# Performance work log

Measured on AMD Instinct MI355X. Metric: run time of the kernel, lower is better.

The kernel has to match this reference:

```python
import jax, jax.numpy as jnp
import numpy as np

# DeformConv (RegSeg): offset conv + mask conv (sigmoid) + modulated deformable conv v2
STRIDE = 1
PAD = 1
DIL = 1
G = 1          # deformable_groups
KH, KW = 3, 3


def _conv(x, w, b):
    # standard NCHW conv, stride/pad/dilation of the module
    y = jax.lax.conv_general_dilated(
        x, w, window_strides=(STRIDE, STRIDE),
        padding=((PAD, PAD), (PAD, PAD)), rhs_dilation=(DIL, DIL),
        dimension_numbers=("NCHW", "OIHW", "NCHW"))
    return y + b[None, :, None, None]


def _deform_conv2d(x, offset, mask, w, b):
    # torchvision DeformConv2d (modulated, v2) semantics
    B, C, H, W = x.shape
    O = w.shape[0]
    K = KH * KW
    Ho = (H + 2 * PAD - DIL * (KH - 1) - 1) // STRIDE + 1
    Wo = (W + 2 * PAD - DIL * (KW - 1) - 1) // STRIDE + 1
    Cg = C // G

    # base sampling grid: p0 + p_k
    ky = jnp.repeat(jnp.arange(KH), KW) * DIL            # [K]
    kx = jnp.tile(jnp.arange(KW), KH) * DIL              # [K]
    oy = jnp.arange(Ho) * STRIDE - PAD                   # [Ho]
    ox = jnp.arange(Wo) * STRIDE - PAD                   # [Wo]
    base_y = (ky[:, None, None] + oy[None, :, None]).astype(x.dtype)  # [K,Ho,1]
    base_x = (kx[:, None, None] + ox[None, None, :]).astype(x.dtype)  # [K,1,Wo]

    off = offset.reshape(B, G, K, 2, Ho, Wo)             # channel layout: g, k, (dy,dx)
    py = base_y[None, None] + off[:, :, :, 0]            # [B,G,K,Ho,Wo]
    px = base_x[None, None] + off[:, :, :, 1]
    m = mask.reshape(B, G, K, Ho, Wo)

    imgf = x.reshape(B * G, Cg, H * W)
    y0 = jnp.floor(py).astype(jnp.int32)
    x0 = jnp.floor(px).astype(jnp.int32)
    ly = py - y0.astype(x.dtype)
    lx = px - x0.astype(x.dtype)

    def corner(iy, ix, wgt):
        # zero-padded bilinear corner: out-of-bounds corners contribute 0
        valid = (iy >= 0) & (iy < H) & (ix >= 0) & (ix < W)
        idx = (jnp.clip(iy, 0, H - 1) * W + jnp.clip(ix, 0, W - 1)).reshape(B * G, -1)
        g = jax.vmap(lambda im, ii: im[:, ii])(imgf, idx)            # [B*G,Cg,K*Ho*Wo]
        g = g.reshape(B, G, Cg, K, Ho, Wo)
        return g * (wgt * valid.astype(x.dtype))[:, :, None]          # [B,G,Cg,K,Ho,Wo]

    val = (corner(y0,     x0,     (1 - ly) * (1 - lx))
         + corner(y0,     x0 + 1, (1 - ly) * lx)
         + corner(y0 + 1, x0,     ly * (1 - lx))
         + corner(y0 + 1, x0 + 1, ly * lx))
    val = val * m[:, :, None]                                         # modulation

    wr = w.reshape(O, G, Cg, K)
    out = jnp.einsum("bgckpq,ogck->bopq", val, wr) + b[None, :, None, None]
    return out


def setup_inputs() -> dict:
    key = jax.random.key(0)
    ks = jax.random.split(key, 8)
    B, C, H, W, O = 4, 128, 96, 96, 128
    K = KH * KW
    fan = 1.0 / np.sqrt(C * K)
    return {
        "x":        jax.random.normal(ks[0], (B, C, H, W), jnp.float32),
        "x2":       jax.random.normal(ks[1], (B, C, H, W), jnp.float32),
        "offset_w": jax.random.normal(ks[2], (2 * G * K, C, KH, KW), jnp.float32) * 0.01,
        "offset_b": jax.random.normal(ks[3], (2 * G * K,), jnp.float32) * 0.01,
        "mask_w":   jax.random.normal(ks[4], (G * K, C, KH, KW), jnp.float32) * 0.05,
        "mask_b":   jnp.zeros((G * K,), jnp.float32),
        "deform_w": jax.random.normal(ks[5], (O, C, KH, KW), jnp.float32) * fan,
        "deform_b": jax.random.normal(ks[6], (O,), jnp.float32) * fan,
    }


def reference(x, x2, offset_w, offset_b, mask_w, mask_b, deform_w, deform_b):
    offset = _conv(x2, offset_w, offset_b)
    mask = jax.nn.sigmoid(_conv(x2, mask_w, mask_b))
    return _deform_conv2d(x, offset, mask, deform_w, deform_b)
```

## Files before the change

### kernel.cpp

```cpp
#include <hip/hip_runtime.h>

#define CIN   128
#define HH    96
#define WW    96
#define OUTC  128
#define HWSZ  9216
#define KK    9
#define KTOT  1152

typedef __bf16 bf16x8 __attribute__((ext_vector_type(8)));
typedef float  f32x4  __attribute__((ext_vector_type(4)));

__device__ __forceinline__ unsigned short f2bf(float f) {
  unsigned u = __builtin_bit_cast(unsigned, f);
  u += 0x7fffu + ((u >> 16) & 1u);
  return (unsigned short)(u >> 16);
}
__device__ __forceinline__ float bf2f_lo(unsigned w) {
  unsigned u = w << 16;
  return __builtin_bit_cast(float, u);
}
__device__ __forceinline__ float bf2f_hi(unsigned w) {
  unsigned u = w & 0xffff0000u;
  return __builtin_bit_cast(float, u);
}
__device__ __forceinline__ unsigned pack_bf(float v0, float v1) {
  unsigned u0 = __builtin_bit_cast(unsigned, v0) + 0x8000u;
  unsigned u1 = __builtin_bit_cast(unsigned, v1) + 0x8000u;
  return __builtin_amdgcn_perm(u1, u0, 0x07060302u);
}

#define WT2B_O 147456
#define BIAS_O 184320
#define XN_O   184384
#define X2N_O  (184384 + 4718592)

__global__ __launch_bounds__(256) void prep_all(
    const float* __restrict__ x, const float* __restrict__ x2,
    const float* __restrict__ offw, const float* __restrict__ maskw,
    const float* __restrict__ defw, const float* __restrict__ offb,
    const float* __restrict__ maskb, void* __restrict__ wsv) {
  int bid = blockIdx.x;
  int t = threadIdx.x;
  if (bid < 1152) {
    __shared__ unsigned short tile[64][138];
    int tsel = bid / 576;
    int rem = bid - tsel * 576;
    int b = rem / 144;
    int hw0 = (rem % 144) * 64;
    const float* src = tsel ? x2 : x;
    unsigned short* dst = (unsigned short*)wsv + (tsel ? X2N_O : XN_O);
    int px = t & 63, cg = t >> 6;
#pragma unroll
    for (int q = 0; q < 16; ++q) {
      int c = cg * 32 + 2 * q;
      float f0 = src[((size_t)(b * CIN + c))     * HWSZ + hw0 + px];
      float f1 = src[((size_t)(b * CIN + c + 1)) * HWSZ + hw0 + px];
      *(unsigned*)&tile[px][c] = pack_bf(f0, f1);
    }
    __syncthreads();
    unsigned* drow = (unsigned*)(dst + ((size_t)(b * HWSZ + hw0)) * 128);
#pragma unroll
    for (int k = 0; k < 16; ++k) {
      int e = t + 256 * k;
      int pxx = e >> 6, j = e & 63;
      unsigned v = *(const unsigned*)&tile[pxx][2 * j];
      drow[(size_t)pxx * 64 + j] = v;
    }
    return;
  }
  unsigned short* wtb  = (unsigned short*)wsv;
  unsigned short* wt2b = wtb + WT2B_O;
  float* bias32 = (float*)(wtb + BIAS_O);
  int idx = (bid - 1152) * 256 + t;
  if (idx < OUTC * KTOT) {
    int o = idx / KTOT, r = idx - o * KTOT;
    int c = r / KK, tap = r - c * KK;
    wtb[o * KTOT + tap * 128 + c] = f2bf(defw[idx]);
  } else if (idx < OUTC * KTOT + 32 * KTOT) {
    int j = idx - OUTC * KTOT;
    int oc = j / KTOT, r = j - oc * KTOT;
    int c = r / KK, tap = r - c * KK;
    float v = 0.f;
    if (oc < 18)      v = offw[j];
    else if (oc < 27) v = maskw[j - 18 * KTOT];
    wt2b[oc * KTOT + tap * 128 + c] = f2bf(v);
  } else if (idx < OUTC * KTOT + 32 * KTOT + 32) {
    int j = idx - OUTC * KTOT - 32 * KTOT;
    float v = 0.f;
    if (j < 18) v = offb[j]; else if (j < 27) v = maskb[j - 18];
    bias32[j] = v;
  }
}

__global__ __launch_bounds__(256, 3) void fused(
    const float* __restrict__ defb, const void* __restrict__ wsv,
    float* __restrict__ out) {
  const unsigned short* wtb  = (const unsigned short*)wsv;
  const unsigned short* wt2b = wtb + WT2B_O;
  const float* bias32 = (const float*)(wtb + BIAS_O);
  const unsigned short* xn  = wtb + XN_O;
  const unsigned short* x2n = wtb + X2N_O;

  __shared__ unsigned bw[64 * 68];
  __shared__ unsigned short val[64][136];
  __shared__ float om[32][68];
  __shared__ unsigned sidxw[KK * 4 * 64];

  int t = threadIdx.x;
  int w = t >> 6;
  int l15 = t & 15, quad = (t >> 4) & 3;
  int rb = blockIdx.x;
  int bid = (rb & 7) * 72 + (rb >> 3);
  int b = bid / 144;
  int pblk = (bid % 144) * 64;

  int phg[4], pwg[4];
#pragma unroll
  for (int G = 0; G < 4; ++G) {
    int p = pblk + w * 16 + G * 4 + quad;
    phg[G] = p / WW;
    pwg[G] = p - phg[G] * WW;
  }

  f32x4 oa0 = {0.f, 0.f, 0.f, 0.f};
  f32x4 oa1 = {0.f, 0.f, 0.f, 0.f};
  const unsigned short* x2nb = x2n + ((size_t)b * HWSZ) * 128;
  for (int tap = 0; tap < KK; ++tap) {
    int ky = tap / 3 - 1, kx = tap % 3 - 1;
    uint4 vG[4];
#pragma unroll
    for (int G = 0; G < 4; ++G) {
      int y = phg[G] + ky, xx = pwg[G] + kx;
      bool ok = ((unsigned)y < HH) && ((unsigned)xx < WW);
      int pos = ok ? (y * WW + xx) : 0;
      uint4 v = *(const uint4*)(x2nb + ((size_t)pos << 7) + l15 * 8);
      vG[G] = ok ? v : make_uint4(0u, 0u, 0u, 0u);
    }
#pragma unroll
    for (int j = 0; j < 2; ++j) {
      int cc = t + 256 * j;
      int row = cc >> 4, c16 = cc & 15;
      *(uint4*)&bw[row * 68 + c16 * 4] =
          *(const uint4*)(wt2b + (size_t)row * KTOT + tap * 128 + c16 * 8);
    }
#pragma unroll
    for (int G = 0; G < 4; ++G)
      *(uint4*)&val[w * 16 + G * 4 + quad][l15 * 8] = vG[G];
    __syncthreads();
#pragma unroll
    for (int ks = 0; ks < 4; ++ks) {
      bf16x8 af = *(const bf16x8*)&val[w * 16 + l15][ks * 32 + quad * 8];
      bf16x8 b0 = *(const bf16x8*)&bw[(size_t)l15 * 68 + ks * 16 + quad * 4];
      bf16x8 b1 = *(const bf16x8*)&bw[(size_t)(l15 + 16) * 68 + ks * 16 + quad * 4];
      oa0 = __builtin_amdgcn_mfma_f32_16x16x32_bf16(af, b0, oa0, 0, 0, 0);
      oa1 = __builtin_amdgcn_mfma_f32_16x16x32_bf16(af, b1, oa1, 0, 0, 0);
    }
    __syncthreads();
  }
#pragma unroll
  for (int nt = 0; nt < 2; ++nt) {
    f32x4 a = nt ? oa1 : oa0;
    int oc = nt * 16 + l15;
    float bia = bias32[oc];
#pragma unroll
    for (int r = 0; r < 4; ++r)
      om[oc][w * 16 + quad * 4 + r] = a[r] + bia;
  }
  __syncthreads();

  for (int e = t; e < KK * 64; e += 256) {
    int tap = e >> 6, pp = e & 63;
    int gp2 = pblk + pp;
    int h = gp2 / WW, ww_ = gp2 % WW;
    float dy = om[2 * tap][pp], dx = om[2 * tap + 1][pp];
    float mr = om[18 + tap][pp];
    float m = 1.f / (1.f + __expf(-mr));
    float py  = (float)(h + tap / 3 - 1) + dy;
    float pxx = (float)(ww_ + tap % 3 - 1) + dx;
    float y0f = floorf(py), x0f = floorf(pxx);
    int y0 = (int)y0f, x0 = (int)x0f;
    float ly = py - y0f, lx = pxx - x0f;
    int y1 = y0 + 1, x1 = x0 + 1;
    bool vy0 = (unsigned)y0 < HH, vy1 = (unsigned)y1 < HH;
    bool vx0 = (unsigned)x0 < WW, vx1 = (unsigned)x1 < WW;
    int cy0 = min(max(y0, 0), HH - 1), cy1 = min(max(y1, 0), HH - 1);
    int cx0 = min(max(x0, 0), WW - 1), cx1 = min(max(x1, 0), WW - 1);
    unsigned i00 = cy0 * WW + cx0, i01 = cy0 * WW + cx1;
    unsigned i10 = cy1 * WW + cx0, i11 = cy1 * WW + cx1;
    float w00 = (vy0 && vx0) ? m * (1.f - ly) * (1.f - lx) : 0.f;
    float w01 = (vy0 && vx1) ? m * (1.f - ly) * lx         : 0.f;
    float w10 = (vy1 && vx0) ? m * ly * (1.f - lx)         : 0.f;
    float w11 = (vy1 && vx1) ? m * ly * lx                 : 0.f;
    sidxw[(tap * 4 + 0) * 64 + pp] = i00 | ((unsigned)f2bf(w00) << 16);
    sidxw[(tap * 4 + 1) * 64 + pp] = i01 | ((unsigned)f2bf(w01) << 16);
    sidxw[(tap * 4 + 2) * 64 + pp] = i10 | ((unsigned)f2bf(w10) << 16);
    sidxw[(tap * 4 + 3) * 64 + pp] = i11 | ((unsigned)f2bf(w11) << 16);
  }
  __syncthreads();

  f32x4 acc[8];
#pragma unroll
  for (int nt = 0; nt < 8; ++nt) acc[nt] = (f32x4){0.f, 0.f, 0.f, 0.f};
  const unsigned short* xnb = xn + ((size_t)b * HWSZ) * 128;

  for (int tap = 0; tap < KK; ++tap) {
    unsigned sw[4][4];
#pragma unroll
    for (int cr = 0; cr < 4; ++cr)
#pragma unroll
      for (int G = 0; G < 4; ++G)
        sw[cr][G] = sidxw[(tap * 4 + cr) * 64 + w * 16 + G * 4 + quad];
    uint4 v[4][4];
#pragma unroll
    for (int G = 0; G < 4; ++G)
#pragma unroll
      for (int cr = 0; cr < 4; ++cr)
        v[cr][G] = *(const uint4*)(xnb + ((size_t)(sw[cr][G] & 0xffffu) << 7) + l15 * 8);
#pragma unroll
    for (int G = 0; G < 4; ++G) {
      float f[8];
#pragma unroll
      for (int j = 0; j < 8; ++j) f[j] = 0.f;
#pragma unroll
      for (int cr = 0; cr < 4; ++cr) {
        float wc = bf2f_hi(sw[cr][G]);
        const unsigned* a = (const unsigned*)&v[cr][G];
#pragma unroll
        for (int j = 0; j < 4; ++j) {
          f[2 * j]     += wc * bf2f_lo(a[j]);
          f[2 * j + 1] += wc * bf2f_hi(a[j]);
        }
      }
      unsigned od[4];
#pragma unroll
      for (int j = 0; j < 4; ++j) od[j] = pack_bf(f[2 * j], f[2 * j + 1]);
      *(uint4*)&val[w * 16 + G * 4 + quad][l15 * 8] =
          make_uint4(od[0], od[1], od[2], od[3]);
    }
#pragma unroll
    for (int j = 0; j < 4; ++j) {
      int cc = t + 256 * j;
      int row = cc >> 4, c16 = cc & 15;
      *(uint4*)&bw[row * 68 + c16 * 4] =
          *(const uint4*)(wtb + (size_t)row * KTOT + tap * 128 + c16 * 8);
    }
    __syncthreads();
    bf16x8 af[4];
#pragma unroll
    for (int ks = 0; ks < 4; ++ks)
      af[ks] = *(const bf16x8*)&val[w * 16 + l15][ks * 32 + quad * 8];
#pragma unroll
    for (int ks = 0; ks < 4; ++ks)
#pragma unroll
      for (int nt = 0; nt < 4; ++nt) {
        bf16x8 bb = *(const bf16x8*)&bw[(size_t)(nt * 16 + l15) * 68 + ks * 16 + quad * 4];
        acc[nt] = __builtin_amdgcn_mfma_f32_16x16x32_bf16(af[ks], bb, acc[nt], 0, 0, 0);
      }
    __syncthreads();
#pragma unroll
    for (int j = 0; j < 4; ++j) {
      int cc = t + 256 * j;
      int row = cc >> 4, c16 = cc & 15;
      *(uint4*)&bw[row * 68 + c16 * 4] =
          *(const uint4*)(wtb + (size_t)(64 + row) * KTOT + tap * 128 + c16 * 8);
    }
    __syncthreads();
#pragma unroll
    for (int ks = 0; ks < 4; ++ks)
#pragma unroll
      for (int nt = 0; nt < 4; ++nt) {
        bf16x8 bb = *(const bf16x8*)&bw[(size_t)(nt * 16 + l15) * 68 + ks * 16 + quad * 4];
        acc[4 + nt] = __builtin_amdgcn_mfma_f32_16x16x32_bf16(af[ks], bb, acc[4 + nt], 0, 0, 0);
      }
    __syncthreads();
  }

  for (int r = 0; r < 4; ++r) {
    f32x4 a0 = acc[2 * r], a1 = acc[2 * r + 1];
    float db0 = defb[r * 32 + l15];
    float db1 = defb[r * 32 + 16 + l15];
    if (r) __syncthreads();
#pragma unroll
    for (int reg = 0; reg < 4; ++reg) {
      om[l15]     [w * 16 + quad * 4 + reg] = a0[reg] + db0;
      om[16 + l15][w * 16 + quad * 4 + reg] = a1[reg] + db1;
    }
    __syncthreads();
    int row = t >> 4;
    int col4 = (t & 15) * 4;
#pragma unroll
    for (int hrow = 0; hrow < 2; ++hrow) {
      int rr = row + hrow * 16;
      float4 vv = *(float4*)&om[rr][col4];
      *(float4*)&out[((size_t)b * OUTC + r * 32 + rr) * HWSZ + pblk + col4] = vv;
    }
  }
}

extern "C" void kernel_launch(void* const* d_in, const int* in_sizes, int n_in,
                              void* d_out, int out_size, void* d_ws, size_t ws_size,
                              hipStream_t stream) {
  const float* x     = (const float*)d_in[0];
  const float* x2    = (const float*)d_in[1];
  const float* offw  = (const float*)d_in[2];
  const float* offb  = (const float*)d_in[3];
  const float* maskw = (const float*)d_in[4];
  const float* maskb = (const float*)d_in[5];
  const float* defw  = (const float*)d_in[6];
  const float* defb  = (const float*)d_in[7];
  float* out = (float*)d_out;

  hipLaunchKernelGGL(prep_all, dim3(1873), dim3(256), 0, stream,
                     x, x2, offw, maskw, defw, offb, maskb, d_ws);
  hipLaunchKernelGGL(fused, dim3(576), dim3(256), 0, stream, defb, d_ws, out);
}
```

Measured before the change: 145.5 us.

## Pre-swizzle weights into MFMA fragment order and load B directly from global

The prep kernel now stores the deform and offset/mask weights in a layout that matches the MFMA B-operand fragment, so each lane reads its bf16x8 straight from global memory (via L1/L2) instead of staging weights through shared memory. This removes the bw LDS buffer, its store loops and several __syncthreads per tap in both the offset conv and the deform GEMM. The val tile is padded to 144 columns. The tradeoff is more global/L2 load traffic per wave, since each of the 4 waves reloads the same weights, with latency exposed directly ahead of the MFMAs. Freeing the LDS could raise occupancy.

```diff
diff --git a/kernel.cpp b/kernel.cpp
--- a/kernel.cpp
+++ b/kernel.cpp
@@ -30,7 +30,7 @@
   return __builtin_amdgcn_perm(u1, u0, 0x07060302u);
 }
 
-#define WT2B_O 147456
+#define WT2T_O 147456
 #define BIAS_O 184320
 #define XN_O   184384
 #define X2N_O  (184384 + 4718592)
@@ -69,22 +69,28 @@
     }
     return;
   }
-  unsigned short* wtb  = (unsigned short*)wsv;
-  unsigned short* wt2b = wtb + WT2B_O;
-  float* bias32 = (float*)(wtb + BIAS_O);
+  unsigned short* wtt  = (unsigned short*)wsv;
+  unsigned short* wt2t = wtt + WT2T_O;
+  float* bias32 = (float*)(wtt + BIAS_O);
   int idx = (bid - 1152) * 256 + t;
   if (idx < OUTC * KTOT) {
     int o = idx / KTOT, r = idx - o * KTOT;
     int c = r / KK, tap = r - c * KK;
-    wtb[o * KTOT + tap * 128 + c] = f2bf(defw[idx]);
+    int nt = o >> 4, l15o = o & 15;
+    int ks = c >> 5, quad = (c >> 3) & 3, j = c & 7;
+    wtt[(size_t)(((tap * 4 + ks) * 8 + nt) * 64 + quad * 16 + l15o) * 8 + j] =
+        f2bf(defw[idx]);
   } else if (idx < OUTC * KTOT + 32 * KTOT) {
-    int j = idx - OUTC * KTOT;
-    int oc = j / KTOT, r = j - oc * KTOT;
+    int jj = idx - OUTC * KTOT;
+    int oc = jj / KTOT, r = jj - oc * KTOT;
     int c = r / KK, tap = r - c * KK;
     float v = 0.f;
-    if (oc < 18)      v = offw[j];
-    else if (oc < 27) v = maskw[j - 18 * KTOT];
-    wt2b[oc * KTOT + tap * 128 + c] = f2bf(v);
+    if (oc < 18)      v = offw[jj];
+    else if (oc < 27) v = maskw[jj - 18 * KTOT];
+    int nt2 = oc >> 4, l15o = oc & 15;
+    int ks = c >> 5, quad = (c >> 3) & 3, j = c & 7;
+    wt2t[(size_t)(((tap * 4 + ks) * 2 + nt2) * 64 + quad * 16 + l15o) * 8 + j] =
+        f2bf(v);
   } else if (idx < OUTC * KTOT + 32 * KTOT + 32) {
     int j = idx - OUTC * KTOT - 32 * KTOT;
     float v = 0.f;
@@ -96,20 +102,20 @@
 __global__ __launch_bounds__(256, 3) void fused(
     const float* __restrict__ defb, const void* __restrict__ wsv,
     float* __restrict__ out) {
-  const unsigned short* wtb  = (const unsigned short*)wsv;
-  const unsigned short* wt2b = wtb + WT2B_O;
-  const float* bias32 = (const float*)(wtb + BIAS_O);
-  const unsigned short* xn  = wtb + XN_O;
-  const unsigned short* x2n = wtb + X2N_O;
-
-  __shared__ unsigned bw[64 * 68];
-  __shared__ unsigned short val[64][136];
+  const unsigned short* wtt  = (const unsigned short*)wsv;
+  const unsigned short* wt2t = wtt + WT2T_O;
+  const float* bias32 = (const float*)(wtt + BIAS_O);
+  const unsigned short* xn  = wtt + XN_O;
+  const unsigned short* x2n = wtt + X2N_O;
+
+  __shared__ unsigned short val[64][144];
   __shared__ float om[32][68];
   __shared__ unsigned sidxw[KK * 4 * 64];
 
   int t = threadIdx.x;
   int w = t >> 6;
-  int l15 = t & 15, quad = (t >> 4) & 3;
+  int l = t & 63;
+  int l15 = l & 15, quad = l >> 4;
   int rb = blockIdx.x;
   int bid = (rb & 7) * 72 + (rb >> 3);
   int b = bid / 144;
@@ -128,35 +134,24 @@
   const unsigned short* x2nb = x2n + ((size_t)b * HWSZ) * 128;
   for (int tap = 0; tap < KK; ++tap) {
     int ky = tap / 3 - 1, kx = tap % 3 - 1;
-    uint4 vG[4];
 #pragma unroll
     for (int G = 0; G < 4; ++G) {
       int y = phg[G] + ky, xx = pwg[G] + kx;
       bool ok = ((unsigned)y < HH) && ((unsigned)xx < WW);
       int pos = ok ? (y * WW + xx) : 0;
       uint4 v = *(const uint4*)(x2nb + ((size_t)pos << 7) + l15 * 8);
-      vG[G] = ok ? v : make_uint4(0u, 0u, 0u, 0u);
-    }
-#pragma unroll
-    for (int j = 0; j < 2; ++j) {
-      int cc = t + 256 * j;
-      int row = cc >> 4, c16 = cc & 15;
-      *(uint4*)&bw[row * 68 + c16 * 4] =
-          *(const uint4*)(wt2b + (size_t)row * KTOT + tap * 128 + c16 * 8);
-    }
-#pragma unroll
-    for (int G = 0; G < 4; ++G)
-      *(uint4*)&val[w * 16 + G * 4 + quad][l15 * 8] = vG[G];
-    __syncthreads();
+      if (!ok) v = make_uint4(0u, 0u, 0u, 0u);
+      *(uint4*)&val[w * 16 + G * 4 + quad][l15 * 8] = v;
+    }
 #pragma unroll
     for (int ks = 0; ks < 4; ++ks) {
       bf16x8 af = *(const bf16x8*)&val[w * 16 + l15][ks * 32 + quad * 8];
-      bf16x8 b0 = *(const bf16x8*)&bw[(size_t)l15 * 68 + ks * 16 + quad * 4];
-      bf16x8 b1 = *(const bf16x8*)&bw[(size_t)(l15 + 16) * 68 + ks * 16 + quad * 4];
+      const unsigned short* bp = wt2t + (size_t)(((tap * 4 + ks) * 2) * 64 + l) * 8;
+      bf16x8 b0 = *(const bf16x8*)bp;
+      bf16x8 b1 = *(const bf16x8*)(bp + 64 * 8);
       oa0 = __builtin_amdgcn_mfma_f32_16x16x32_bf16(af, b0, oa0, 0, 0, 0);
       oa1 = __builtin_amdgcn_mfma_f32_16x16x32_bf16(af, b1, oa1, 0, 0, 0);
     }
-    __syncthreads();
   }
 #pragma unroll
   for (int nt = 0; nt < 2; ++nt) {
@@ -238,42 +233,19 @@
       *(uint4*)&val[w * 16 + G * 4 + quad][l15 * 8] =
           make_uint4(od[0], od[1], od[2], od[3]);
     }
-#pragma unroll
-    for (int j = 0; j < 4; ++j) {
-      int cc = t + 256 * j;
-      int row = cc >> 4, c16 = cc & 15;
-      *(uint4*)&bw[row * 68 + c16 * 4] =
-          *(const uint4*)(wtb + (size_t)row * KTOT + tap * 128 + c16 * 8);
-    }
-    __syncthreads();
     bf16x8 af[4];
 #pragma unroll
     for (int ks = 0; ks < 4; ++ks)
       af[ks] = *(const bf16x8*)&val[w * 16 + l15][ks * 32 + quad * 8];
 #pragma unroll
-    for (int ks = 0; ks < 4; ++ks)
-#pragma unroll
-      for (int nt = 0; nt < 4; ++nt) {
-        bf16x8 bb = *(const bf16x8*)&bw[(size_t)(nt * 16 + l15) * 68 + ks * 16 + quad * 4];
+    for (int ks = 0; ks < 4; ++ks) {
+      const unsigned short* bp = wtt + (size_t)(((tap * 4 + ks) * 8) * 64 + l) * 8;
+#pragma unroll
+      for (int nt = 0; nt < 8; ++nt) {
+        bf16x8 bb = *(const bf16x8*)(bp + (size_t)nt * 64 * 8);
         acc[nt] = __builtin_amdgcn_mfma_f32_16x16x32_bf16(af[ks], bb, acc[nt], 0, 0, 0);
       }
-    __syncthreads();
-#pragma unroll
-    for (int j = 0; j < 4; ++j) {
-      int cc = t + 256 * j;
-      int row = cc >> 4, c16 = cc & 15;
-      *(uint4*)&bw[row * 68 + c16 * 4] =
-          *(const uint4*)(wtb + (size_t)(64 + row) * KTOT + tap * 128 + c16 * 8);
-    }
-    __syncthreads();
-#pragma unroll
-    for (int ks = 0; ks < 4; ++ks)
-#pragma unroll
-      for (int nt = 0; nt < 4; ++nt) {
-        bf16x8 bb = *(const bf16x8*)&bw[(size_t)(nt * 16 + l15) * 68 + ks * 16 + quad * 4];
-        acc[4 + nt] = __builtin_amdgcn_mfma_f32_16x16x32_bf16(af[ks], bb, acc[4 + nt], 0, 0, 0);
-      }
-    __syncthreads();
+    }
   }
 
   for (int r = 0; r < 4; ++r) {
```

Measured after the change: 165.2 us. 1.14x slower.
